# Performance work log

Hardware: AMD Instinct MI355X
Metric: run time of the kernel (lower is better)

## Reference

```python
import jax, jax.numpy as jnp
import numpy as np

CTX = (16, 16)          # rel_pos_ctx_size
N_HEADS = 12
HEAD_DIM = 64           # emb_dim // n_heads


def _make_rel_pos_ids(ctx):
    # Faithful replication of the torch buffer construction.
    rge = [2 * s - 1 for s in ctx]
    coords = np.stack(np.meshgrid(*[np.arange(s) for s in ctx], indexing='ij'))  # [2, *ctx]
    coords = coords.reshape(len(ctx), -1)                                        # [2, n]
    rel = coords[:, :, None] - coords[:, None, :]                                # [2, n, n]
    rel = rel.reshape(len(ctx), -1)                                              # [2, n*n]
    rel = rel + (np.array(ctx)[:, None] - 1)
    ids = np.ravel_multi_index(tuple(rel), tuple(rge))                           # [n*n]
    return jnp.asarray(ids, dtype=jnp.int32)


def setup_inputs() -> dict:
    key = jax.random.key(0)
    ks = jax.random.split(key, 6)
    b, n, e = 128, 256, 768
    std_in = 1.0 / np.sqrt(e)
    return {
        'x': jax.random.normal(ks[0], (b, n, e), jnp.float32),
        'W_qkv': jax.random.normal(ks[1], (e, 3 * e), jnp.float32) * std_in,
        'b_qkv': jax.random.normal(ks[2], (3 * e,), jnp.float32) * 0.02,
        'W_out': jax.random.normal(ks[3], (e, e), jnp.float32) * std_in,
        'b_out': jax.random.normal(ks[4], (e,), jnp.float32) * 0.02,
        'rel_bias_table': jax.random.normal(ks[5], ((2 * CTX[0] - 1) * (2 * CTX[1] - 1), N_HEADS), jnp.float32) * 0.02,
        'rel_pos_ids': _make_rel_pos_ids(CTX),
    }


def reference(x, W_qkv, b_qkv, W_out, b_out, rel_bias_table, rel_pos_ids):
    b, n, e = x.shape
    h, d = N_HEADS, HEAD_DIM
    scale = d ** -0.5
    # fused qkv projection: 'b n (k h d) -> k b h n d'
    qkv = (x @ W_qkv + b_qkv).reshape(b, n, 3, h, d)
    q, k, v = (jnp.transpose(qkv, (2, 0, 3, 1, 4))[i] for i in range(3))  # each [b h n d]
    # gathered relative-position bias: [n*n, h] -> [h, n, n]
    bias = rel_bias_table[rel_pos_ids].reshape(n, n, h).transpose(2, 0, 1)
    scores = jnp.einsum('bhnd,bhmd->bhnm', q, k) * scale + bias
    attn = jax.nn.softmax(scores, axis=-1)
    out = jnp.einsum('bhnm,bhmd->bhnd', attn, v)
    out = out.transpose(0, 2, 1, 3).reshape(b, n, e)  # 'b h n d -> b n (h d)'
    return out @ W_out + b_out
```

## Files before the change

### kernel.cpp

```cpp
#include <hip/hip_runtime.h>
#include <cstdint>
#include <cstddef>

typedef __bf16 bf16x8 __attribute__((ext_vector_type(8)));
typedef __bf16 bf16x4 __attribute__((ext_vector_type(4)));
typedef float f32x4 __attribute__((ext_vector_type(4)));
static_assert(sizeof(bf16x8) == 16, "bf16x8 must be 16B");
static_assert(sizeof(bf16x4) == 8, "bf16x4 must be 8B");
static_assert(sizeof(f32x4) == 16, "f32x4 must be 16B");

#define MFMA16(a, b, c) __builtin_amdgcn_mfma_f32_16x16x32_bf16((a), (b), (c), 0, 0, 0)
#define SBAR() __builtin_amdgcn_s_barrier()
#define LGKM0() asm volatile("s_waitcnt lgkmcnt(0)" ::: "memory")
#define VMCNT(n_) asm volatile("s_waitcnt vmcnt(" #n_ ")" ::: "memory")

__device__ __forceinline__ void gload_lds16(const void* g, void* l) {
  __builtin_amdgcn_global_load_lds(
      (const __attribute__((address_space(1))) void*)g,
      (__attribute__((address_space(3))) void*)l, 16, 0, 0);
}

__global__ __launch_bounds__(256) void conv_x_kernel(const float* __restrict__ in,
                                                     __bf16* __restrict__ out) {
  size_t i = ((size_t)blockIdx.x * 256 + threadIdx.x) * 4;
  const float4 v = *(const float4*)(in + i);
  out[i + 0] = (__bf16)v.x;
  out[i + 1] = (__bf16)v.y;
  out[i + 2] = (__bf16)v.z;
  out[i + 3] = (__bf16)v.w;
}

__global__ __launch_bounds__(256) void transpose_conv_kernel(const float* __restrict__ in,
                                                             __bf16* __restrict__ out,
                                                             int K, int N) {
  __shared__ float tile[32][33];
  const int n0 = blockIdx.x * 32, k0 = blockIdx.y * 32;
  const int tx = threadIdx.x, ty = threadIdx.y;
#pragma unroll
  for (int i = 0; i < 4; ++i)
    tile[ty * 4 + i][tx] = in[(size_t)(k0 + ty * 4 + i) * N + n0 + tx];
  __syncthreads();
#pragma unroll
  for (int i = 0; i < 4; ++i)
    out[(size_t)(n0 + ty * 4 + i) * K + k0 + tx] = (__bf16)tile[tx][ty * 4 + i];
}

__global__ __launch_bounds__(256) void bias_gather_kernel(const float* __restrict__ table,
                                                          const int* __restrict__ ids,
                                                          float* __restrict__ biasT) {
  const int idx = blockIdx.x * 256 + threadIdx.x;
  const int h = idx >> 16, ji = idx & 65535;
  const int j = ji >> 8, i = ji & 255;
  biasT[idx] = table[ids[i * 256 + j] * 12 + h];
}

template <int MODE, int NT>
__global__ __launch_bounds__(512, 2) void gemm8_kernel(const __bf16* __restrict__ A,
                                                       const __bf16* __restrict__ Bt,
                                                       const float* __restrict__ bias,
                                                       void* __restrict__ out0,
                                                       __bf16* __restrict__ kbuf,
                                                       const int M, const int N, const int K) {
  constexpr bool TRANS = (MODE != 2);
  __shared__ __align__(16) __bf16 smem[65536];
  const int tid = threadIdx.x;
  const int lane = tid & 63, w = tid >> 6;
  const int m16 = lane & 15, q4 = lane >> 4;
  const int wm = w & 1, wn = w >> 1;

  const int nwg = NT * (M >> 8);
  const int chunk = nwg >> 3;
  const int id = blockIdx.x;
  const int wg = (id & 7) * chunk + (id >> 3);
  const int mi = wg / NT, ni = wg - mi * NT;
  const int m0 = mi << 8, n0 = ni << 8;

  const int srow = w * 8 + (lane >> 3);
  const int sg = ((lane & 7) ^ (srow & 7)) * 8;
  const __bf16* ag = A + (size_t)(m0 + srow) * K + sg;
  const __bf16* bg = Bt + (size_t)(n0 + srow) * K + sg;
  const int dstw = w * 512;

  const int g0 = (q4 ^ (m16 & 7)) * 8;
  const int g1 = ((4 + q4) ^ (m16 & 7)) * 8;
  const int abase = (wm * 128 + m16) * 64;
  const int bbase = 16384 + (wn * 64 + m16) * 64;

  const int nt = K >> 6;

#define STAGE(T_, mat_, h_)                                                        \
  do {                                                                             \
    const __bf16* s_ = ((mat_) ? bg : ag) + (size_t)(T_)*64 + (size_t)(h_)*128 * K; \
    __bf16* d_ = &smem[((T_)&1) * 32768 + (mat_)*16384 + (h_)*8192 + dstw];        \
    gload_lds16(s_, d_);                                                           \
    gload_lds16(s_ + (size_t)64 * K, d_ + 4096);                                   \
  } while (0)

#define MM(a_, b_, c_) (TRANS ? MFMA16((b_), (a_), (c_)) : MFMA16((a_), (b_), (c_)))

  STAGE(0, 0, 0);
  STAGE(0, 0, 1);
  STAGE(0, 1, 0);
  STAGE(0, 1, 1);
  STAGE(1, 0, 0);
  VMCNT(2);
  SBAR();

  f32x4 acc[8][4] = {};
  for (int T = 0; T < nt; ++T) {
    const int base = (T & 1) * 32768;
    bf16x8 a[4][2], b0[2][2], b1[2][2];

#pragma unroll
    for (int fm = 0; fm < 4; ++fm) {
      a[fm][0] = *(const bf16x8*)&smem[base + abase + fm * 1024 + g0];
      a[fm][1] = *(const bf16x8*)&smem[base + abase + fm * 1024 + g1];
    }
#pragma unroll
    for (int fn = 0; fn < 2; ++fn) {
      b0[fn][0] = *(const bf16x8*)&smem[base + bbase + fn * 1024 + g0];
      b0[fn][1] = *(const bf16x8*)&smem[base + bbase + fn * 1024 + g1];
    }
    if (T + 1 < nt) STAGE(T + 1, 0, 1);
    SBAR();
    LGKM0();
    __builtin_amdgcn_s_setprio(1);
#pragma unroll
    for (int kh = 0; kh < 2; ++kh)
#pragma unroll
      for (int fm = 0; fm < 4; ++fm)
#pragma unroll
        for (int fn = 0; fn < 2; ++fn)
          acc[fm][fn] = MM(a[fm][kh], b0[fn][kh], acc[fm][fn]);
    __builtin_amdgcn_s_setprio(0);
    SBAR();

#pragma unroll
    for (int fn = 0; fn < 2; ++fn) {
      b1[fn][0] = *(const bf16x8*)&smem[base + bbase + 2048 + fn * 1024 + g0];
      b1[fn][1] = *(const bf16x8*)&smem[base + bbase + 2048 + fn * 1024 + g1];
    }
    if (T + 1 < nt) {
      STAGE(T + 1, 1, 0);
      STAGE(T + 1, 1, 1);
    }
    SBAR();
    LGKM0();
    __builtin_amdgcn_s_setprio(1);
#pragma unroll
    for (int kh = 0; kh < 2; ++kh)
#pragma unroll
      for (int fm = 0; fm < 4; ++fm)
#pragma unroll
        for (int fn = 0; fn < 2; ++fn)
          acc[fm][2 + fn] = MM(a[fm][kh], b1[fn][kh], acc[fm][2 + fn]);
    __builtin_amdgcn_s_setprio(0);
    SBAR();

#pragma unroll
    for (int fm = 0; fm < 4; ++fm) {
      a[fm][0] = *(const bf16x8*)&smem[base + abase + 4096 + fm * 1024 + g0];
      a[fm][1] = *(const bf16x8*)&smem[base + abase + 4096 + fm * 1024 + g1];
    }
    SBAR();
    LGKM0();
    __builtin_amdgcn_s_setprio(1);
#pragma unroll
    for (int kh = 0; kh < 2; ++kh)
#pragma unroll
      for (int fm = 0; fm < 4; ++fm)
#pragma unroll
        for (int fn = 0; fn < 2; ++fn)
          acc[4 + fm][2 + fn] = MM(a[fm][kh], b1[fn][kh], acc[4 + fm][2 + fn]);
    __builtin_amdgcn_s_setprio(0);
    SBAR();

    if (T + 2 < nt) {
      STAGE(T + 2, 0, 0);
      VMCNT(2);
    } else if (T + 1 < nt) {
      VMCNT(0);
    }
    SBAR();
    __builtin_amdgcn_s_setprio(1);
#pragma unroll
    for (int kh = 0; kh < 2; ++kh)
#pragma unroll
      for (int fm = 0; fm < 4; ++fm)
#pragma unroll
        for (int fn = 0; fn < 2; ++fn)
          acc[4 + fm][fn] = MM(a[fm][kh], b0[fn][kh], acc[4 + fm][fn]);
    __builtin_amdgcn_s_setprio(0);
    SBAR();
  }
#undef STAGE
#undef MM

  const int gmb = m0 + wm * 128;
  const int gnb = n0 + wn * 64;

  if (MODE == 0) {
    __bf16* qb = (__bf16*)out0;
    const int which = (gnb >= 768);
    __bf16* dst = which ? kbuf : qb;
    const float qscale = which ? 1.0f : 0.125f;
    const int bi = gmb >> 8;
    const int tokb = gmb & 255;
#pragma unroll
    for (int fn = 0; fn < 4; ++fn) {
      const int gn0 = gnb + fn * 16 + q4 * 4;
      const f32x4 bn = *(const f32x4*)&bias[gn0];
      const int rem0 = gn0 - which * 768;
      const int hh = rem0 >> 6, dd0 = rem0 & 63;
      __bf16* basep = dst + ((size_t)bi * 12 + hh) * 16384 + dd0;
#pragma unroll
      for (int fm = 0; fm < 8; ++fm) {
        const int tok = tokb + fm * 16 + m16;
        bf16x4 pk;
#pragma unroll
        for (int r = 0; r < 4; ++r) pk[r] = (__bf16)((acc[fm][fn][r] + bn[r]) * qscale);
        *(bf16x4*)(basep + (size_t)tok * 64) = pk;
      }
    }
  } else if (MODE == 2) {
    __bf16* vt = (__bf16*)out0;
    const int bi = gmb >> 8;
    const int tokb = gmb & 255;
#pragma unroll
    for (int fn = 0; fn < 4; ++fn) {
      const int gn = gnb + fn * 16 + m16;
      const float bn = bias[gn];
      const int hh = gn >> 6, dd = gn & 63;
      __bf16* basep = vt + (((size_t)bi * 12 + hh) * 64 + dd) * 256;
#pragma unroll
      for (int fm = 0; fm < 8; ++fm) {
        const int tok0 = tokb + fm * 16 + q4 * 4;
        bf16x4 pk;
#pragma unroll
        for (int r = 0; r < 4; ++r) pk[r] = (__bf16)(acc[fm][fn][r] + bn);
        *(bf16x4*)(basep + tok0) = pk;
      }
    }
  } else {
    float* out = (float*)out0;
#pragma unroll
    for (int fn = 0; fn < 4; ++fn) {
      const int gn0 = gnb + fn * 16 + q4 * 4;
      const f32x4 bn = *(const f32x4*)&bias[gn0];
#pragma unroll
      for (int fm = 0; fm < 8; ++fm) {
        const int gm = gmb + fm * 16 + m16;
        f32x4 v;
#pragma unroll
        for (int r = 0; r < 4; ++r) v[r] = acc[fm][fn][r] + bn[r];
        *(f32x4*)(out + (size_t)gm * N + gn0) = v;
      }
    }
  }
}

__global__ __launch_bounds__(512, 4) void attn_kernel(const __bf16* __restrict__ qb,
                                                      const __bf16* __restrict__ kb,
                                                      const __bf16* __restrict__ vtb,
                                                      const float* __restrict__ biasT,
                                                      __bf16* __restrict__ o_ws) {
  __shared__ __bf16 klds[256 * 64];
  __shared__ __bf16 vlds[64 * 256];
  const int tid = threadIdx.x;
  const int lane = tid & 63, w = tid >> 6;
  const int m16 = lane & 15, q4 = lane >> 4;
  const int b = blockIdx.x, h = blockIdx.y;
  const size_t bh = (size_t)b * 12 + h;
  const __bf16* Q = qb + bh * (256 * 64);
  const __bf16* Kp = kb + bh * (256 * 64);
  const __bf16* Vt = vtb + bh * (64 * 256);
  const float* BhT = biasT + (size_t)h * 65536;
  const int qbase = blockIdx.z * 128;
  const int qrow0 = qbase + w * 16;

#pragma unroll
  for (int i = 0; i < 4; ++i) {
    const int row = w * 32 + i * 8 + (lane >> 3);
    const int col = ((lane & 7) ^ (row & 7)) * 8;
    gload_lds16(Kp + (size_t)row * 64 + col, &klds[(w * 32 + i * 8) * 64]);
  }
#pragma unroll
  for (int i = 0; i < 4; ++i) {
    const int row = w * 8 + i * 2 + (lane >> 5);
    const int g = lane & 31;
    const int gp = (g & 24) | ((g & 7) ^ (row & 7));
    gload_lds16(Vt + (size_t)row * 256 + gp * 8, &vlds[(w * 8 + i * 2) * 256]);
  }

  bf16x8 qf[2];
#pragma unroll
  for (int t = 0; t < 2; ++t)
    qf[t] = *(const bf16x8*)(Q + (size_t)(qrow0 + m16) * 64 + t * 32 + q4 * 8);

  __syncthreads();

  f32x4 s[16];
#pragma unroll
  for (int c = 0; c < 16; ++c) {
    const int krow = c * 16 + m16;
    const bf16x8 kf0 = *(const bf16x8*)&klds[krow * 64 + ((q4 ^ (m16 & 7)) * 8)];
    const bf16x8 kf1 = *(const bf16x8*)&klds[krow * 64 + (((4 + q4) ^ (m16 & 7)) * 8)];
    f32x4 z = {0.f, 0.f, 0.f, 0.f};
    z = MFMA16(qf[0], kf0, z);
    s[c] = MFMA16(qf[1], kf1, z);
  }

#pragma unroll
  for (int c = 0; c < 16; ++c) {
    const f32x4 bv = *(const f32x4*)&BhT[(size_t)(c * 16 + m16) * 256 + qrow0 + q4 * 4];
    s[c] += bv;
  }

  float linv[4];
#pragma unroll
  for (int r = 0; r < 4; ++r) {
    float mx = s[0][r];
#pragma unroll
    for (int c = 1; c < 16; ++c) mx = fmaxf(mx, s[c][r]);
    mx = fmaxf(mx, __shfl_xor(mx, 1));
    mx = fmaxf(mx, __shfl_xor(mx, 2));
    mx = fmaxf(mx, __shfl_xor(mx, 4));
    mx = fmaxf(mx, __shfl_xor(mx, 8));
    float sum = 0.f;
#pragma unroll
    for (int c = 0; c < 16; ++c) {
      const float p = exp2f((s[c][r] - mx) * 1.4426950408889634f);
      s[c][r] = p;
      sum += p;
    }
    sum += __shfl_xor(sum, 1);
    sum += __shfl_xor(sum, 2);
    sum += __shfl_xor(sum, 4);
    sum += __shfl_xor(sum, 8);
    linv[r] = 1.f / sum;
  }

  __syncthreads();

  f32x4 o[4] = {};
  __bf16* P = &klds[w * 1152];
#pragma unroll
  for (int ch = 0; ch < 4; ++ch) {
#pragma unroll
    for (int cc = 0; cc < 4; ++cc)
#pragma unroll
      for (int r = 0; r < 4; ++r)
        P[(q4 * 4 + r) * 72 + cc * 16 + m16] = (__bf16)s[ch * 4 + cc][r];
#pragma unroll
    for (int kt = 0; kt < 2; ++kt) {
      const bf16x8 pf = *(const bf16x8*)(P + m16 * 72 + kt * 32 + q4 * 8);
#pragma unroll
      for (int dt = 0; dt < 4; ++dt) {
        const int vrow = dt * 16 + m16;
        const bf16x8 vf = *(const bf16x8*)&vlds[vrow * 256 + ch * 64 +
                                                (((kt * 4 + q4) ^ (m16 & 7)) * 8)];
        o[dt] = MFMA16(pf, vf, o[dt]);
      }
    }
  }

#pragma unroll
  for (int dt = 0; dt < 4; ++dt)
#pragma unroll
    for (int r = 0; r < 4; ++r) {
      const float v = o[dt][r] * linv[r];
      const size_t row = (size_t)b * 256 + qrow0 + q4 * 4 + r;
      o_ws[row * 768 + h * 64 + dt * 16 + m16] = (__bf16)v;
    }
}

extern "C" void kernel_launch(void* const* d_in, const int* in_sizes, int n_in,
                              void* d_out, int out_size, void* d_ws, size_t ws_size,
                              hipStream_t stream) {
  const float* x = (const float*)d_in[0];
  const float* Wqkv = (const float*)d_in[1];
  const float* bqkv = (const float*)d_in[2];
  const float* Wout = (const float*)d_in[3];
  const float* bout = (const float*)d_in[4];
  const float* table = (const float*)d_in[5];
  const int* ids = (const int*)d_in[6];
  float* out = (float*)d_out;

  char* ws = (char*)d_ws;
  __bf16* xbf = (__bf16*)ws;
  __bf16* wqkvt = (__bf16*)(ws + 50331648);
  __bf16* woutt = (__bf16*)(ws + 53870592);
  __bf16* qbuf = (__bf16*)(ws + 55050240);
  __bf16* kbuf = (__bf16*)(ws + 105381888);
  __bf16* vtbuf = (__bf16*)(ws + 155713536);
  float* biasT = (float*)(ws + 206045184);

  conv_x_kernel<<<24576, 256, 0, stream>>>(x, xbf);
  transpose_conv_kernel<<<dim3(72, 24), dim3(32, 8), 0, stream>>>(Wqkv, wqkvt, 768, 2304);
  transpose_conv_kernel<<<dim3(24, 24), dim3(32, 8), 0, stream>>>(Wout, woutt, 768, 768);
  bias_gather_kernel<<<3072, 256, 0, stream>>>(table, ids, biasT);
  gemm8_kernel<0, 6><<<768, 512, 0, stream>>>(xbf, wqkvt, bqkv, qbuf, kbuf,
                                              32768, 1536, 768);
  gemm8_kernel<2, 3><<<384, 512, 0, stream>>>(xbf, wqkvt + (size_t)1536 * 768,
                                              bqkv + 1536, vtbuf, nullptr,
                                              32768, 768, 768);
  attn_kernel<<<dim3(128, 12, 2), 512, 0, stream>>>(qbuf, kbuf, vtbuf, biasT, xbf );
  gemm8_kernel<1, 3><<<384, 512, 0, stream>>>(xbf, woutt, bout, out, nullptr,
                                              32768, 768, 768);
}
```

Before: 502.4 us.

## Stage GEMM epilogues through swizzled LDS for coalesced 16-byte global stores

The GEMM epilogues for the Q/K, V-transposed and output projections now write accumulator fragments into XOR-swizzled shared memory. Each block then re-reads them row-wise and issues full 16-byte coalesced global stores, replacing scattered 8-byte stores. The fp32 output path is staged in two halves so it fits the buffer. The x conversion kernel also packs four bf16 values into one vector store. This adds extra barriers and LDS round-trips to every GEMM tile's epilogue.

```diff
diff --git a/kernel.cpp b/kernel.cpp
--- a/kernel.cpp
+++ b/kernel.cpp
@@ -24,10 +24,12 @@
                                                      __bf16* __restrict__ out) {
   size_t i = ((size_t)blockIdx.x * 256 + threadIdx.x) * 4;
   const float4 v = *(const float4*)(in + i);
-  out[i + 0] = (__bf16)v.x;
-  out[i + 1] = (__bf16)v.y;
-  out[i + 2] = (__bf16)v.z;
-  out[i + 3] = (__bf16)v.w;
+  bf16x4 pk;
+  pk[0] = (__bf16)v.x;
+  pk[1] = (__bf16)v.y;
+  pk[2] = (__bf16)v.z;
+  pk[3] = (__bf16)v.w;
+  *(bf16x4*)(out + i) = pk;
 }
 
 __global__ __launch_bounds__(256) void transpose_conv_kernel(const float* __restrict__ in,
@@ -196,65 +198,98 @@
 #undef STAGE
 #undef MM
 
-  const int gmb = m0 + wm * 128;
-  const int gnb = n0 + wn * 64;
+  __syncthreads();
 
   if (MODE == 0) {
-    __bf16* qb = (__bf16*)out0;
-    const int which = (gnb >= 768);
-    __bf16* dst = which ? kbuf : qb;
+    const int which = (n0 >= 768);
     const float qscale = which ? 1.0f : 0.125f;
-    const int bi = gmb >> 8;
-    const int tokb = gmb & 255;
+    char* eb = (char*)smem;
 #pragma unroll
     for (int fn = 0; fn < 4; ++fn) {
-      const int gn0 = gnb + fn * 16 + q4 * 4;
-      const f32x4 bn = *(const f32x4*)&bias[gn0];
-      const int rem0 = gn0 - which * 768;
-      const int hh = rem0 >> 6, dd0 = rem0 & 63;
-      __bf16* basep = dst + ((size_t)bi * 12 + hh) * 16384 + dd0;
+      const int nloc = wn * 64 + fn * 16 + q4 * 4;
+      const f32x4 bn = *(const f32x4*)&bias[n0 + nloc];
+      const int cb = nloc * 2;
+      const int slot = cb >> 4;
+      const int half8 = cb & 15;
 #pragma unroll
       for (int fm = 0; fm < 8; ++fm) {
-        const int tok = tokb + fm * 16 + m16;
+        const int tok = wm * 128 + fm * 16 + m16;
         bf16x4 pk;
 #pragma unroll
         for (int r = 0; r < 4; ++r) pk[r] = (__bf16)((acc[fm][fn][r] + bn[r]) * qscale);
-        *(bf16x4*)(basep + (size_t)tok * 64) = pk;
+        *(bf16x4*)(eb + tok * 512 + ((slot ^ (tok & 7)) << 4) + half8) = pk;
       }
     }
+    __syncthreads();
+    const int bi = m0 >> 8;
+    const int nrel0 = n0 - which * 768;
+    __bf16* dst = (which ? kbuf : (__bf16*)out0) + (size_t)bi * 12 * 16384;
+#pragma unroll
+    for (int pass = 0; pass < 16; ++pass) {
+      const int tokr = pass * 16 + (tid >> 5);
+      const int slot = tid & 31;
+      const bf16x8 vv = *(const bf16x8*)(eb + tokr * 512 + ((slot ^ (tokr & 7)) << 4));
+      const int nr = nrel0 + slot * 8;
+      *(bf16x8*)(dst + (size_t)(nr >> 6) * 16384 + (size_t)tokr * 64 + (nr & 63)) = vv;
+    }
   } else if (MODE == 2) {
+    char* eb = (char*)smem;
+#pragma unroll
+    for (int fn = 0; fn < 4; ++fn) {
+      const int nloc = wn * 64 + fn * 16 + m16;
+      const float bn = bias[n0 + nloc];
+#pragma unroll
+      for (int fm = 0; fm < 8; ++fm) {
+        const int tcb = (wm * 128 + fm * 16 + q4 * 4) * 2;
+        const int slot = tcb >> 4;
+        const int half8 = tcb & 15;
+        bf16x4 pk;
+#pragma unroll
+        for (int r = 0; r < 4; ++r) pk[r] = (__bf16)(acc[fm][fn][r] + bn);
+        *(bf16x4*)(eb + nloc * 512 + ((slot ^ (nloc & 7)) << 4) + half8) = pk;
+      }
+    }
+    __syncthreads();
+    const int bi = m0 >> 8;
     __bf16* vt = (__bf16*)out0;
-    const int bi = gmb >> 8;
-    const int tokb = gmb & 255;
-#pragma unroll
-    for (int fn = 0; fn < 4; ++fn) {
-      const int gn = gnb + fn * 16 + m16;
-      const float bn = bias[gn];
-      const int hh = gn >> 6, dd = gn & 63;
-      __bf16* basep = vt + (((size_t)bi * 12 + hh) * 64 + dd) * 256;
-#pragma unroll
-      for (int fm = 0; fm < 8; ++fm) {
-        const int tok0 = tokb + fm * 16 + q4 * 4;
-        bf16x4 pk;
-#pragma unroll
-        for (int r = 0; r < 4; ++r) pk[r] = (__bf16)(acc[fm][fn][r] + bn);
-        *(bf16x4*)(basep + tok0) = pk;
+#pragma unroll
+    for (int pass = 0; pass < 16; ++pass) {
+      const int nr = pass * 16 + (tid >> 5);
+      const int slot = tid & 31;
+      const bf16x8 vv = *(const bf16x8*)(eb + nr * 512 + ((slot ^ (nr & 7)) << 4));
+      const int ng = n0 + nr;
+      *(bf16x8*)(vt + (((size_t)bi * 12 + (ng >> 6)) * 64 + (ng & 63)) * 256 + slot * 8) = vv;
+    }
+  } else {
+    char* ef = (char*)smem;
+    float* out = (float*)out0;
+#pragma unroll
+    for (int half = 0; half < 2; ++half) {
+      if ((wn >> 1) == half) {
+#pragma unroll
+        for (int fn = 0; fn < 4; ++fn) {
+          const int nl = (wn & 1) * 64 + fn * 16 + q4 * 4;
+          const f32x4 bn = *(const f32x4*)&bias[n0 + half * 128 + nl];
+          const int slot = nl >> 2;
+#pragma unroll
+          for (int fm = 0; fm < 8; ++fm) {
+            const int tok = wm * 128 + fm * 16 + m16;
+            f32x4 v;
+#pragma unroll
+            for (int r = 0; r < 4; ++r) v[r] = acc[fm][fn][r] + bn[r];
+            *(f32x4*)(ef + tok * 512 + ((slot ^ (tok & 7)) << 4)) = v;
+          }
+        }
       }
-    }
-  } else {
-    float* out = (float*)out0;
-#pragma unroll
-    for (int fn = 0; fn < 4; ++fn) {
-      const int gn0 = gnb + fn * 16 + q4 * 4;
-      const f32x4 bn = *(const f32x4*)&bias[gn0];
-#pragma unroll
-      for (int fm = 0; fm < 8; ++fm) {
-        const int gm = gmb + fm * 16 + m16;
-        f32x4 v;
-#pragma unroll
-        for (int r = 0; r < 4; ++r) v[r] = acc[fm][fn][r] + bn[r];
-        *(f32x4*)(out + (size_t)gm * N + gn0) = v;
+      __syncthreads();
+#pragma unroll
+      for (int pass = 0; pass < 16; ++pass) {
+        const int tokr = pass * 16 + (tid >> 5);
+        const int slot = tid & 31;
+        const f32x4 vv = *(const f32x4*)(ef + tokr * 512 + ((slot ^ (tokr & 7)) << 4));
+        *(f32x4*)(out + (size_t)(m0 + tokr) * N + n0 + half * 128 + slot * 4) = vv;
       }
+      __syncthreads();
     }
   }
 }
```

Measured after the change: 474.5 us. 5.6% less time.
